# Kernel optimization log

Measured on AMD Instinct MI355X. Metric: run time of the kernel, lower is better.

The kernel has to match this reference:

```python
import jax, jax.numpy as jnp
import numpy as np

N = 50000   # num nodes
E = 800000  # num edges (avg degree 16)
D = 64      # feature dim for input and both layers


def setup_inputs() -> dict:
    key = jax.random.key(0)
    ks = jax.random.split(key, 8)
    x = jax.random.normal(ks[0], (N, D), dtype=jnp.float32)
    edge_index = jax.random.randint(ks[1], (2, E), 0, N, dtype=jnp.int32)
    s = 1.0 / np.sqrt(D)
    # PyG SAGEConv params per layer: lin_l (on aggregated neighbors, with bias),
    # lin_r (on root node, no bias)
    Wl0 = jax.random.uniform(ks[2], (D, D), jnp.float32, -s, s)
    bl0 = jax.random.uniform(ks[3], (D,), jnp.float32, -s, s)
    Wr0 = jax.random.uniform(ks[4], (D, D), jnp.float32, -s, s)
    Wl1 = jax.random.uniform(ks[5], (D, D), jnp.float32, -s, s)
    bl1 = jax.random.uniform(ks[6], (D,), jnp.float32, -s, s)
    Wr1 = jax.random.uniform(ks[7], (D, D), jnp.float32, -s, s)
    return dict(node_features=x, edge_index=edge_index,
                Wl0=Wl0, bl0=bl0, Wr0=Wr0, Wl1=Wl1, bl1=bl1, Wr1=Wr1)


def _sage_conv(x, src, dst, Wl, bl, Wr):
    """PyG SAGEConv (mean aggr) after add_self_loops: mean over neighbors+self."""
    msg = x[src]  # [E, D] irregular gather
    summ = jax.ops.segment_sum(msg, dst, num_segments=x.shape[0]) + x  # self-loop
    deg = jax.ops.segment_sum(jnp.ones(src.shape, x.dtype), dst,
                              num_segments=x.shape[0]) + 1.0
    mean = summ / deg[:, None]
    return mean @ Wl + bl + x @ Wr


def reference(node_features, edge_index, Wl0, bl0, Wr0, Wl1, bl1, Wr1):
    src, dst = edge_index[0], edge_index[1]
    # dropout is a no-op in eval mode; batch_norms are unused in the original forward
    x = jax.nn.relu(_sage_conv(node_features, src, dst, Wl0, bl0, Wr0))
    x = jax.nn.relu(_sage_conv(x, src, dst, Wl1, bl1, Wr1))
    return x
```

## Files before the change

### kernel.cpp

```cpp
#include <hip/hip_runtime.h>
#include <hip/hip_bf16.h>

#define N_NODES 50000
#define N_EDGES 800000
#define FDIM 64
#define NBUCK 196
#define CAP 4608
#define CAP2 5632
#define PAD 16

typedef __attribute__((ext_vector_type(8))) short short8;
typedef __attribute__((ext_vector_type(4))) float f32x4;

__device__ __forceinline__ unsigned f2bf(float f) {
    unsigned u = __float_as_uint(f);
    u += 0x7fffu + ((u >> 16) & 1u);
    return u >> 16;
}
__device__ __forceinline__ float bf2f_lo(unsigned u) { return __uint_as_float(u << 16); }
__device__ __forceinline__ float bf2f_hi(unsigned u) { return __uint_as_float(u & 0xffff0000u); }

__device__ __forceinline__ int excl_scan_256(int v, int* wtot, int* wincl) {
    const int t = threadIdx.x, lane = t & 63, w = t >> 6;
    int sv = v;
#pragma unroll
    for (int off = 1; off < 64; off <<= 1) {
        int u = __shfl_up(sv, off, 64);
        if (lane >= off) sv += u;
    }
    if (lane == 63) wtot[w] = sv;
    __syncthreads();
    if (w == 0 && lane < 4) {
        int incl = 0;
#pragma unroll
        for (int k = 0; k < 4; ++k)
            if (k <= lane) incl += wtot[k];
        wincl[lane] = incl;
    }
    __syncthreads();
    return (w ? wincl[w - 1] : 0) + sv - v;
}

__global__ __launch_bounds__(256)
void preprocess_kernel(const float* __restrict__ x0, unsigned short* __restrict__ x_bf,
                       const float* __restrict__ Wl0, const float* __restrict__ Wr0,
                       const float* __restrict__ Wl1, const float* __restrict__ Wr1,
                       unsigned short* __restrict__ pW,
                       const int* __restrict__ src, const int* __restrict__ dst,
                       int* __restrict__ cur_pad, unsigned* __restrict__ ebuf) {
    const int b = blockIdx.x;
    const int t = threadIdx.x;
    if (b < 3125) {
        int i = (b * 256 + t) * 4;
        float4 v = *(const float4*)(x0 + i);
        uint2 o;
        o.x = f2bf(v.x) | (f2bf(v.y) << 16);
        o.y = f2bf(v.z) | (f2bf(v.w) << 16);
        *(uint2*)(x_bf + i) = o;
    } else if (b < 3129) {
        const float* Wsrc[4] = {Wl0, Wr0, Wl1, Wr1};
        const float* W = Wsrc[b - 3125];
        unsigned short* P = pW + (b - 3125) * FDIM * FDIM;
        for (int idx = t; idx < FDIM * FDIM; idx += 256) {
            int j = idx & 7;
            int lane = (idx >> 3) & 63;
            int g = idx >> 9;
            int ct = g >> 1, kk = g & 1;
            int k = kk * 32 + ((lane >> 4) & 3) * 8 + j;
            int col = ct * 16 + (lane & 15);
            P[idx] = (unsigned short)f2bf(W[k * FDIM + col]);
        }
    } else {
        __shared__ int h[NBUCK];
        __shared__ int base[NBUCK];
        if (t < NBUCK) h[t] = 0;
        __syncthreads();

        int e0 = (b - 3129) * 1024 + t * 4;
        int bk0 = -1, bk1 = -1, bk2 = -1, bk3 = -1;
        int rk0 = 0, rk1 = 0, rk2 = 0, rk3 = 0;
        unsigned pk0 = 0, pk1 = 0, pk2 = 0, pk3 = 0;
        const bool ok = (e0 < N_EDGES);
        if (ok) {
            int4 s4 = *(const int4*)(src + e0);
            int4 d4 = *(const int4*)(dst + e0);
            bk0 = d4.x >> 8; pk0 = ((unsigned)d4.x << 16) | (unsigned)s4.x;
            bk1 = d4.y >> 8; pk1 = ((unsigned)d4.y << 16) | (unsigned)s4.y;
            bk2 = d4.z >> 8; pk2 = ((unsigned)d4.z << 16) | (unsigned)s4.z;
            bk3 = d4.w >> 8; pk3 = ((unsigned)d4.w << 16) | (unsigned)s4.w;
            rk0 = atomicAdd(&h[bk0], 1);
            rk1 = atomicAdd(&h[bk1], 1);
            rk2 = atomicAdd(&h[bk2], 1);
            rk3 = atomicAdd(&h[bk3], 1);
        }
        __syncthreads();
        if (t < NBUCK) {
            int c = h[t];
            base[t] = c ? (t * CAP + atomicAdd(&cur_pad[t * PAD], c)) : 0;
        }
        __syncthreads();
        if (ok) {
            ebuf[base[bk0] + rk0] = pk0;
            ebuf[base[bk1] + rk1] = pk1;
            ebuf[base[bk2] + rk2] = pk2;
            ebuf[base[bk3] + rk3] = pk3;
        }
    }
}

__global__ __launch_bounds__(256)
void bucket_csr_kernel(const unsigned* __restrict__ ebuf, const int* __restrict__ cur_pad,
                       int* __restrict__ row_start, unsigned short* __restrict__ degs,
                       unsigned short* __restrict__ csr) {
    __shared__ int cnt[256];
    __shared__ int cur[256];
    __shared__ int wtot[4], wincl[4];
    __shared__ __align__(16) unsigned short sC[CAP2];
    const int b = blockIdx.x;
    const int t = threadIdx.x;
    const int s = b * CAP;
    const int m = cur_pad[b * PAD];
    const int s2 = b * CAP2;

    cnt[t] = 0;
    __syncthreads();

    unsigned pk[18];
#pragma unroll
    for (int k = 0; k < 18; ++k) {
        int i = k * 256 + t;
        if (i < m) {
            pk[k] = ebuf[s + i];
            atomicAdd(&cnt[(pk[k] >> 16) & 255], 1);
        }
    }
    __syncthreads();

    int c = cnt[t];
    int c8 = (c + 7) & ~7;
    int ex = excl_scan_256(c8, wtot, wincl);
    cur[t] = ex;
    int node = b * 256 + t;
    if (node < N_NODES) {
        row_start[node] = s2 + ex;
        degs[node] = (unsigned short)c;
    }
    __syncthreads();

#pragma unroll
    for (int k = 0; k < 18; ++k) {
        int i = k * 256 + t;
        if (i < m) {
            int pos = atomicAdd(&cur[(pk[k] >> 16) & 255], 1);
            sC[pos] = (unsigned short)pk[k];
        }
    }
    __syncthreads();

    const int tot = wincl[3];
    for (int i = t * 8; i < tot; i += 2048)
        *(uint4*)(csr + s2 + i) = *(const uint4*)(&sC[i]);
}

template <bool OUT_BF16>
__global__ __launch_bounds__(128)
void sage_fused_kernel(const unsigned short* __restrict__ xb,
                       const int* __restrict__ row_start,
                       const unsigned short* __restrict__ degs,
                       const unsigned short* __restrict__ csr,
                       const unsigned short* __restrict__ pWl,
                       const float* __restrict__ bl,
                       const unsigned short* __restrict__ pWr,
                       float* __restrict__ out_f32,
                       unsigned short* __restrict__ out_bf) {
    __shared__ __align__(16) unsigned short smean[16][FDIM];
    __shared__ __align__(16) unsigned short sxs[16][FDIM];

    const int w = threadIdx.x >> 6;
    const int lane = threadIdx.x & 63;
    const int slot = lane >> 3;
    const int c = lane & 7;
    const int base = blockIdx.x * 16;
    const int r = w * 8 + slot;
    const int n = base + r;

    uint4 sv = *(const uint4*)(xb + (size_t)n * FDIM + c * 8);

    const int rs = row_start[n];
    const int deg = degs[n];
    const int po = (c ^ (r & 7)) * 8;

    *(uint4*)(&sxs[r][po]) = sv;
    float s0 = bf2f_lo(sv.x), s1 = bf2f_hi(sv.x);
    float s2 = bf2f_lo(sv.y), s3 = bf2f_hi(sv.y);
    float s4 = bf2f_lo(sv.z), s5 = bf2f_hi(sv.z);
    float s6 = bf2f_lo(sv.w), s7 = bf2f_hi(sv.w);

#define ACC(v_) do {                                   \
        s0 += bf2f_lo(v_.x); s1 += bf2f_hi(v_.x);      \
        s2 += bf2f_lo(v_.y); s3 += bf2f_hi(v_.y);      \
        s4 += bf2f_lo(v_.z); s5 += bf2f_hi(v_.z);      \
        s6 += bf2f_lo(v_.w); s7 += bf2f_hi(v_.w);      \
    } while (0)

    int idx = rs;
    int rem = deg;
    uint4 iA = *(const uint4*)(csr + idx);
    while (rem >= 8) {
        int a0 = iA.x & 0xffff, a1 = iA.x >> 16;
        int a2 = iA.y & 0xffff, a3 = iA.y >> 16;
        int a4 = iA.z & 0xffff, a5 = iA.z >> 16;
        int a6 = iA.w & 0xffff, a7 = iA.w >> 16;
        uint4 v0 = *(const uint4*)(xb + (size_t)a0 * FDIM + c * 8);
        uint4 v1 = *(const uint4*)(xb + (size_t)a1 * FDIM + c * 8);
        uint4 v2 = *(const uint4*)(xb + (size_t)a2 * FDIM + c * 8);
        uint4 v3 = *(const uint4*)(xb + (size_t)a3 * FDIM + c * 8);
        uint4 v4 = *(const uint4*)(xb + (size_t)a4 * FDIM + c * 8);
        uint4 v5 = *(const uint4*)(xb + (size_t)a5 * FDIM + c * 8);
        uint4 v6 = *(const uint4*)(xb + (size_t)a6 * FDIM + c * 8);
        uint4 v7 = *(const uint4*)(xb + (size_t)a7 * FDIM + c * 8);
        if (rem > 8)
            iA = *(const uint4*)(csr + idx + 8);
        ACC(v0); ACC(v1); ACC(v2); ACC(v3);
        ACC(v4); ACC(v5); ACC(v6); ACC(v7);
        idx += 8; rem -= 8;
    }
    if (rem > 0) {
        int a[8];
        a[0] = iA.x & 0xffff; a[1] = iA.x >> 16;
        a[2] = iA.y & 0xffff; a[3] = iA.y >> 16;
        a[4] = iA.z & 0xffff; a[5] = iA.z >> 16;
        a[6] = iA.w & 0xffff; a[7] = iA.w >> 16;
#pragma unroll
        for (int k = 0; k < 8; ++k) {
            if (k < rem) {
                uint4 v = *(const uint4*)(xb + (size_t)a[k] * FDIM + c * 8);
                ACC(v);
            }
        }
    }
#undef ACC

    const float inv = 1.0f / (float)(deg + 1);
    uint4 o;
    o.x = f2bf(s0 * inv) | (f2bf(s1 * inv) << 16);
    o.y = f2bf(s2 * inv) | (f2bf(s3 * inv) << 16);
    o.z = f2bf(s4 * inv) | (f2bf(s5 * inv) << 16);
    o.w = f2bf(s6 * inv) | (f2bf(s7 * inv) << 16);
    *(uint4*)(&smean[r][po]) = o;
    __syncthreads();

    const int qq = lane >> 4;
    const int rr = lane & 15;

    short8 am0 = *(const short8*)(&smean[rr][((0 + qq) ^ (rr & 7)) * 8]);
    short8 am1 = *(const short8*)(&smean[rr][((4 + qq) ^ (rr & 7)) * 8]);
    short8 ax0 = *(const short8*)(&sxs[rr][((0 + qq) ^ (rr & 7)) * 8]);
    short8 ax1 = *(const short8*)(&sxs[rr][((4 + qq) ^ (rr & 7)) * 8]);

    const short8* pl = (const short8*)pWl;
    const short8* pr = (const short8*)pWr;

#pragma unroll
    for (int tk = 0; tk < 2; ++tk) {
        const int ct = w * 2 + tk;
        short8 bl0v = pl[(ct * 2 + 0) * 64 + lane];
        short8 bl1v = pl[(ct * 2 + 1) * 64 + lane];
        short8 br0v = pr[(ct * 2 + 0) * 64 + lane];
        short8 br1v = pr[(ct * 2 + 1) * 64 + lane];

        float b = bl[ct * 16 + rr];
        f32x4 acc = {b, b, b, b};
        acc = __builtin_amdgcn_mfma_f32_16x16x32_bf16(am0, bl0v, acc, 0, 0, 0);
        acc = __builtin_amdgcn_mfma_f32_16x16x32_bf16(am1, bl1v, acc, 0, 0, 0);
        acc = __builtin_amdgcn_mfma_f32_16x16x32_bf16(ax0, br0v, acc, 0, 0, 0);
        acc = __builtin_amdgcn_mfma_f32_16x16x32_bf16(ax1, br1v, acc, 0, 0, 0);

#pragma unroll
        for (int reg = 0; reg < 4; ++reg) {
            int node = base + qq * 4 + reg;
            float v = fmaxf(acc[reg], 0.0f);
            if (OUT_BF16) out_bf[(size_t)node * FDIM + ct * 16 + rr] = (unsigned short)f2bf(v);
            else          out_f32[(size_t)node * FDIM + ct * 16 + rr] = v;
        }
    }
}

extern "C" void kernel_launch(void* const* d_in, const int* in_sizes, int n_in,
                              void* d_out, int out_size, void* d_ws, size_t ws_size,
                              hipStream_t stream) {
    const float* x0  = (const float*)d_in[0];
    const int*   ei  = (const int*)d_in[1];
    const float* Wl0 = (const float*)d_in[2];
    const float* bl0 = (const float*)d_in[3];
    const float* Wr0 = (const float*)d_in[4];
    const float* Wl1 = (const float*)d_in[5];
    const float* bl1 = (const float*)d_in[6];
    const float* Wr1 = (const float*)d_in[7];
    float* out = (float*)d_out;

    const int* src = ei;
    const int* dst = ei + N_EDGES;

    int* cur_pad    = (int*)d_ws;
    int* row_start  = cur_pad + 3136;
    unsigned short* degs = (unsigned short*)(row_start + 50000);
    unsigned* ebuf  = (unsigned*)(degs + 50000);
    unsigned short* csr_u16 = (unsigned short*)(ebuf + NBUCK * CAP);
    unsigned short* x_bf = csr_u16 + (NBUCK * CAP2 + 1024);
    unsigned short* h_bf = x_bf + (size_t)N_NODES * FDIM;
    unsigned short* pW   = h_bf + (size_t)N_NODES * FDIM;

    hipMemsetAsync(cur_pad, 0, 3136 * sizeof(int), stream);
    preprocess_kernel<<<3911, 256, 0, stream>>>(x0, x_bf, Wl0, Wr0, Wl1, Wr1,
                                                pW, src, dst, cur_pad, ebuf);
    bucket_csr_kernel<<<NBUCK, 256, 0, stream>>>(ebuf, cur_pad, row_start, degs, csr_u16);

    sage_fused_kernel<true><<<N_NODES / 16, 128, 0, stream>>>(
        x_bf, row_start, degs, csr_u16, pW + 0 * FDIM * FDIM, bl0,
        pW + 1 * FDIM * FDIM, nullptr, h_bf);
    sage_fused_kernel<false><<<N_NODES / 16, 128, 0, stream>>>(
        h_bf, row_start, degs, csr_u16, pW + 2 * FDIM * FDIM, bl1,
        pW + 3 * FDIM * FDIM, out, nullptr);
}
```

Before: 150.7 us.

## Sort nodes by degree into a permutation to balance per-block gather work

Result: slower. 158.3 us (+5.0%).

```diff
diff --git a/kernel.cpp b/kernel.cpp
--- a/kernel.cpp
+++ b/kernel.cpp
@@ -111,9 +111,10 @@
 __global__ __launch_bounds__(256)
 void bucket_csr_kernel(const unsigned* __restrict__ ebuf, const int* __restrict__ cur_pad,
                        int* __restrict__ row_start, unsigned short* __restrict__ degs,
-                       unsigned short* __restrict__ csr) {
+                       unsigned short* __restrict__ csr, int* __restrict__ ghist) {
     __shared__ int cnt[256];
     __shared__ int cur[256];
+    __shared__ int lh[64];
     __shared__ int wtot[4], wincl[4];
     __shared__ __align__(16) unsigned short sC[CAP2];
     const int b = blockIdx.x;
@@ -123,6 +124,7 @@
     const int s2 = b * CAP2;
 
     cnt[t] = 0;
+    if (t < 64) lh[t] = 0;
     __syncthreads();
 
     unsigned pk[18];
@@ -137,15 +139,21 @@
     __syncthreads();
 
     int c = cnt[t];
+    int node = b * 256 + t;
+    if (node < N_NODES) atomicAdd(&lh[c > 63 ? 63 : c], 1);
     int c8 = (c + 7) & ~7;
     int ex = excl_scan_256(c8, wtot, wincl);
     cur[t] = ex;
-    int node = b * 256 + t;
     if (node < N_NODES) {
         row_start[node] = s2 + ex;
         degs[node] = (unsigned short)c;
     }
     __syncthreads();
+
+    if (t < 64) {
+        int v = lh[t];
+        if (v) atomicAdd(&ghist[t], v);
+    }
 
 #pragma unroll
     for (int k = 0; k < 18; ++k) {
@@ -160,6 +168,36 @@
     const int tot = wincl[3];
     for (int i = t * 8; i < tot; i += 2048)
         *(uint4*)(csr + s2 + i) = *(const uint4*)(&sC[i]);
+}
+
+__global__ __launch_bounds__(256)
+void perm_kernel(const unsigned short* __restrict__ degs,
+                 const int* __restrict__ ghist, int* __restrict__ gcur,
+                 int* __restrict__ perm) {
+    __shared__ int lg[64];
+    __shared__ int lh[64];
+    __shared__ int lcur[64];
+    const int b = blockIdx.x, t = threadIdx.x;
+    if (t < 64) { lg[t] = ghist[t]; lh[t] = 0; }
+    __syncthreads();
+    const int node = b * 256 + t;
+    int bin = 0;
+    if (node < N_NODES) {
+        bin = degs[node]; if (bin > 63) bin = 63;
+        atomicAdd(&lh[bin], 1);
+    }
+    __syncthreads();
+    if (t < 64) {
+        int ex = 0;
+        for (int k = 0; k < t; ++k) ex += lg[k];
+        int cc = lh[t];
+        lcur[t] = ex + (cc ? atomicAdd(&gcur[t], cc) : 0);
+    }
+    __syncthreads();
+    if (node < N_NODES) {
+        int pos = atomicAdd(&lcur[bin], 1);
+        perm[pos] = node;
+    }
 }
 
 template <bool OUT_BF16>
@@ -168,6 +206,7 @@
                        const int* __restrict__ row_start,
                        const unsigned short* __restrict__ degs,
                        const unsigned short* __restrict__ csr,
+                       const int* __restrict__ perm,
                        const unsigned short* __restrict__ pWl,
                        const float* __restrict__ bl,
                        const unsigned short* __restrict__ pWr,
@@ -182,7 +221,7 @@
     const int c = lane & 7;
     const int base = blockIdx.x * 16;
     const int r = w * 8 + slot;
-    const int n = base + r;
+    const int n = perm[base + r];
 
     uint4 sv = *(const uint4*)(xb + (size_t)n * FDIM + c * 8);
 
@@ -258,6 +297,10 @@
     short8 ax0 = *(const short8*)(&sxs[rr][((0 + qq) ^ (rr & 7)) * 8]);
     short8 ax1 = *(const short8*)(&sxs[rr][((4 + qq) ^ (rr & 7)) * 8]);
 
+    int nd[4];
+#pragma unroll
+    for (int reg = 0; reg < 4; ++reg) nd[reg] = perm[base + qq * 4 + reg];
+
     const short8* pl = (const short8*)pWl;
     const short8* pr = (const short8*)pWr;
 
@@ -278,10 +321,9 @@
 
 #pragma unroll
         for (int reg = 0; reg < 4; ++reg) {
-            int node = base + qq * 4 + reg;
             float v = fmaxf(acc[reg], 0.0f);
-            if (OUT_BF16) out_bf[(size_t)node * FDIM + ct * 16 + rr] = (unsigned short)f2bf(v);
-            else          out_f32[(size_t)node * FDIM + ct * 16 + rr] = v;
+            if (OUT_BF16) out_bf[(size_t)nd[reg] * FDIM + ct * 16 + rr] = (unsigned short)f2bf(v);
+            else          out_f32[(size_t)nd[reg] * FDIM + ct * 16 + rr] = v;
         }
     }
 }
@@ -303,23 +345,28 @@
     const int* dst = ei + N_EDGES;
 
     int* cur_pad    = (int*)d_ws;
-    int* row_start  = cur_pad + 3136;
-    unsigned short* degs = (unsigned short*)(row_start + 50000);
+    int* ghist      = cur_pad + 3136;
+    int* gcur       = cur_pad + 3200;
+    int* row_start  = cur_pad + 3264;
+    int* perm       = row_start + 50000;
+    unsigned short* degs = (unsigned short*)(perm + 50000);
     unsigned* ebuf  = (unsigned*)(degs + 50000);
     unsigned short* csr_u16 = (unsigned short*)(ebuf + NBUCK * CAP);
     unsigned short* x_bf = csr_u16 + (NBUCK * CAP2 + 1024);
     unsigned short* h_bf = x_bf + (size_t)N_NODES * FDIM;
     unsigned short* pW   = h_bf + (size_t)N_NODES * FDIM;
 
-    hipMemsetAsync(cur_pad, 0, 3136 * sizeof(int), stream);
+    hipMemsetAsync(cur_pad, 0, 3264 * sizeof(int), stream);
     preprocess_kernel<<<3911, 256, 0, stream>>>(x0, x_bf, Wl0, Wr0, Wl1, Wr1,
                                                 pW, src, dst, cur_pad, ebuf);
-    bucket_csr_kernel<<<NBUCK, 256, 0, stream>>>(ebuf, cur_pad, row_start, degs, csr_u16);
+    bucket_csr_kernel<<<NBUCK, 256, 0, stream>>>(ebuf, cur_pad, row_start, degs,
+                                                 csr_u16, ghist);
+    perm_kernel<<<NBUCK, 256, 0, stream>>>(degs, ghist, gcur, perm);
 
     sage_fused_kernel<true><<<N_NODES / 16, 128, 0, stream>>>(
-        x_bf, row_start, degs, csr_u16, pW + 0 * FDIM * FDIM, bl0,
+        x_bf, row_start, degs, csr_u16, perm, pW + 0 * FDIM * FDIM, bl0,
         pW + 1 * FDIM * FDIM, nullptr, h_bf);
     sage_fused_kernel<false><<<N_NODES / 16, 128, 0, stream>>>(
-        h_bf, row_start, degs, csr_u16, pW + 2 * FDIM * FDIM, bl1,
+        h_bf, row_start, degs, csr_u16, perm, pW + 2 * FDIM * FDIM, bl1,
         pW + 3 * FDIM * FDIM, out, nullptr);
 }
```
